# Optimization experiments

Hardware: AMD Instinct MI355X
Metric: run time of the kernel (lower is better)

Reference implementation:

```python
import jax, jax.numpy as jnp
import numpy as np

SEQ, BATCH, IN_DIM, HID, NQ, TAGS = 2048, 1, 8, 4, 4, 32

# ---- 2x2 gate builders (support batched angle t of shape () or (B,)) ----

def _mat2(a, b, c, d):
    vals = [jnp.asarray(v, jnp.complex64) for v in (a, b, c, d)]
    a, b, c, d = jnp.broadcast_arrays(*vals)
    return jnp.stack([jnp.stack([a, b], -1), jnp.stack([c, d], -1)], -2)

def RZg(t):
    t = jnp.asarray(t, jnp.float32).astype(jnp.complex64)
    return _mat2(jnp.exp(-0.5j * t), 0.0, 0.0, jnp.exp(0.5j * t))

def RYg(t):
    t = jnp.asarray(t, jnp.float32); c = jnp.cos(t / 2); s = jnp.sin(t / 2)
    return _mat2(c, -s, s, c)

def RXg(t):
    t = jnp.asarray(t, jnp.float32); c = jnp.cos(t / 2); s = jnp.sin(t / 2)
    return _mat2(c, -1j * s, -1j * s, c)

def PHg(t):
    t = jnp.asarray(t, jnp.float32)
    return _mat2(jnp.ones_like(t), 0.0, 0.0, jnp.exp(1j * t.astype(jnp.complex64)))

_HAD = jnp.array([[1, 1], [1, -1]], jnp.complex64) / np.float32(np.sqrt(2.0))

# ---- statevector primitives (qubit q little-endian: stride 2^q) ----

def apply_1q(psi, U, q, n):
    B = psi.shape[0]
    psi = psi.reshape(B, 1 << (n - 1 - q), 2, 1 << q)
    if U.ndim == 2:
        out = jnp.einsum('ab,Bxby->Bxay', U, psi)
    else:
        out = jnp.einsum('Bab,Bxby->Bxay', U, psi)
    return out.reshape(B, -1)

def apply_cnot(psi, c, t, n):
    B = psi.shape[0]
    p = psi.reshape((B,) + (2,) * n)
    axc, axt = 1 + (n - 1 - c), 1 + (n - 1 - t)
    p = jnp.moveaxis(p, (axc, axt), (1, 2))
    p = jnp.concatenate([p[:, :1], p[:, 1:, ::-1]], axis=1)  # flip target where control=1
    p = jnp.moveaxis(p, (1, 2), (axc, axt))
    return p.reshape(B, -1)

# ---- QCNN conv / pool two-qubit blocks (faithful to source gate lists) ----

def conv_block(psi, a, b, p, n):
    psi = apply_1q(psi, RZg(-np.pi / 2), b, n)
    psi = apply_cnot(psi, b, a, n)
    psi = apply_1q(psi, RZg(p[0]), a, n)
    psi = apply_1q(psi, RYg(p[1]), b, n)
    psi = apply_cnot(psi, a, b, n)
    psi = apply_1q(psi, RYg(p[2]), b, n)
    psi = apply_cnot(psi, b, a, n)
    psi = apply_1q(psi, RZg(np.pi / 2), a, n)
    return psi

def pool_block(psi, a, b, p, n):
    psi = apply_1q(psi, RZg(-np.pi / 2), b, n)
    psi = apply_cnot(psi, b, a, n)
    psi = apply_1q(psi, RZg(p[0]), a, n)
    psi = apply_1q(psi, RYg(p[1]), b, n)
    psi = apply_cnot(psi, a, b, n)
    psi = apply_1q(psi, RYg(p[2]), b, n)
    return psi

# block wiring exactly as built by conv_layer/pool_layer composed on qubits 0..k
CONV1 = [(0, 1), (2, 3), (4, 5), (6, 7), (1, 2), (3, 4), (5, 6), (7, 0)]
POOL1 = [(0, 4), (1, 5), (2, 6), (3, 7)]
CONV2 = [(0, 1), (2, 3), (1, 2), (3, 0)]
POOL2 = [(0, 2), (1, 3)]
CONV3 = [(0, 1), (1, 0)]
POOL3 = [(0, 1)]

def qcnn_forward(x, w):
    # x: (B,8) inputs, w: (63,) ansatz weights -> (B,) expectation <Z_7>
    B = x.shape[0]
    psi = jnp.zeros((B, 256), jnp.complex64).at[:, 0].set(1.0)
    for q in range(8):  # ZFeatureMap(reps=1): H then P(2*x_q) on each qubit
        psi = apply_1q(psi, _HAD, q, 8)
        psi = apply_1q(psi, PHg(2.0 * x[:, q]), q, 8)
    k = 0
    for blocks, fn in ((CONV1, conv_block), (POOL1, pool_block), (CONV2, conv_block),
                       (POOL2, pool_block), (CONV3, conv_block), (POOL3, pool_block)):
        for (a, b) in blocks:
            psi = fn(psi, a, b, w[k:k + 3], 8)
            k += 3
    probs = psi.real ** 2 + psi.imag ** 2
    # observable 'Z'+'I'*7 in Qiskit big-endian string => Z on qubit 7
    sign7 = 1.0 - 2.0 * ((jnp.arange(256) >> 7) & 1).astype(jnp.float32)
    return probs @ sign7

_SIGNS4 = 1.0 - 2.0 * ((jnp.arange(16)[None, :] >> jnp.arange(4)[:, None]) & 1).astype(jnp.float32)  # (4,16)

def qlayer(angles):
    # angles (B,4): encoder rx + trainable rx fused (RX(a)RX(b)=RX(a+b) on same wire)
    B = angles.shape[0]
    psi = jnp.zeros((B, 16), jnp.complex64).at[:, 0].set(1.0)
    for wq in range(4):
        psi = apply_1q(psi, RXg(angles[:, wq]), wq, 4)
    for (c, t) in ((0, 1), (1, 2), (2, 3), (3, 0)):
        psi = apply_cnot(psi, c, t, 4)
    probs = psi.real ** 2 + psi.imag ** 2
    return probs @ _SIGNS4.T  # (B,4) = <Z_w> per wire

def model_forward(sentence, qcnn_w, Wf, bf, Wi, bi, Wu, bu, Wo, bo, thf, thi, thu, tho, Wt, bt):
    S, B, D = sentence.shape
    q = qcnn_forward(sentence.reshape(S * B, D), qcnn_w).reshape(S, B, 1)
    h0 = jnp.zeros((B, HID), jnp.float32)
    c0 = jnp.zeros((B, HID), jnp.float32)
    Ws = jnp.stack([Wf, Wi, Wu, Wo])        # (4, NQ, 1+HID)
    bs = jnp.stack([bf, bi, bu, bo])        # (4, NQ)
    ths = jnp.stack([thf, thi, thu, tho])   # (4, NQ)

    def step(carry, x):
        h, c = carry
        comb = jnp.concatenate([x, h], axis=1)                         # (B, 1+HID)
        ys = jnp.einsum('gqd,Bd->gBq', Ws, comb) + bs[:, None, :]      # (4,B,NQ)
        z = qlayer((ys + ths[:, None, :]).reshape(4 * B, NQ)).reshape(4, B, NQ)
        f = jax.nn.sigmoid(z[0]); i_ = jax.nn.sigmoid(z[1])
        g = jnp.tanh(z[2]); o = jax.nn.sigmoid(z[3])
        c2 = f * c + i_ * g
        h2 = o * jnp.tanh(c2)
        return (h2, c2), h2

    _, hs = jax.lax.scan(step, (h0, c0), q)    # (S,B,HID)
    logits = hs.reshape(S, -1) @ Wt.T + bt      # batch must be 1 per source view()
    return jax.nn.log_softmax(logits, axis=1)


def setup_inputs() -> dict:
    key = jax.random.key(0)
    ks = jax.random.split(key, 16)
    rn = lambda k, s: jax.random.normal(k, s, jnp.float32)
    return {
        'sentence': rn(ks[0], (SEQ, BATCH, IN_DIM)),
        'qcnn_w': rn(ks[1], (63,)),
        'Wf': rn(ks[2], (NQ, 1 + HID)), 'bf': rn(ks[3], (NQ,)),
        'Wi': rn(ks[4], (NQ, 1 + HID)), 'bi': rn(ks[5], (NQ,)),
        'Wu': rn(ks[6], (NQ, 1 + HID)), 'bu': rn(ks[7], (NQ,)),
        'Wo': rn(ks[8], (NQ, 1 + HID)), 'bo': rn(ks[9], (NQ,)),
        'thf': rn(ks[10], (NQ,)), 'thi': rn(ks[11], (NQ,)),
        'thu': rn(ks[12], (NQ,)), 'tho': rn(ks[13], (NQ,)),
        'Wt': rn(ks[14], (TAGS, HID)), 'bt': rn(ks[15], (TAGS,)),
    }


def reference(sentence, qcnn_w, Wf, bf, Wi, bi, Wu, bu, Wo, bo, thf, thi, thu, tho, Wt, bt):
    return model_forward(sentence, qcnn_w, Wf, bf, Wi, bi, Wu, bu, Wo, bo, thf, thi, thu, tho, Wt, bt)
```

## Files before the change

### kernel.cpp

```cpp
#include <hip/hip_runtime.h>
#include <math.h>


#define MAXS 2048
#define SEG  8
#define WARM 24
#define WIN  (WARM + SEG)

__device__ __align__(16) float g_preT[16 * MAXS];

template <int CTRL>
__device__ __forceinline__ float dppf(float x) {
    return __int_as_float(__builtin_amdgcn_update_dpp(
        0, __float_as_int(x), CTRL, 0xF, 0xF, true));
}
#define QP_1032 0xB1
#define QP_2301 0x4E
#define QP_3210 0x1B
#define ROR4  0x124
#define ROR8  0x128
#define ROR12 0x12C

__device__ __forceinline__ float fastrcp(float x) {
    return __builtin_amdgcn_rcpf(x);
}

constexpr int hf(int m)  { return (m ^ (((m << 1) | (m >> 3)) & 15)) & 15; }
__device__ __forceinline__ int swzi(int i) {
    const int m = (i >> 4) & 15;
    return i ^ m ^ (((m << 1) | (m >> 3)) & 15);
}
constexpr int DM(int a) { return (a < 4) ? (1 << a)
                                         : ((1 << a) ^ hf(1 << (a - 4))); }

constexpr int AQ[21] = {0,2,4,6,1,3,5,7, 0,1,2,3, 0,2,1,3, 0,1, 0,1, 0};
constexpr int BQ[21] = {1,3,5,7,2,4,6,0, 4,5,6,7, 1,3,2,0, 2,3, 1,0, 1};
constexpr int CV[21] = {1,1,1,1,1,1,1,1, 0,0,0,0, 1,1,1,1, 0,0, 1,1, 0};

__device__ __forceinline__ float2 cmulacc(float2 acc, float2 u, float2 a) {
    acc.x = fmaf(u.x, a.x, fmaf(-u.y, a.y, acc.x));
    acc.y = fmaf(u.x, a.y, fmaf( u.y, a.x, acc.y));
    return acc;
}

__global__ __launch_bounds__(256) void qcnn_kernel(
    const float* __restrict__ sent, const float* __restrict__ wpar,
    const float* __restrict__ Wf, const float* __restrict__ bfv,
    const float* __restrict__ Wi, const float* __restrict__ bi,
    const float* __restrict__ Wu, const float* __restrict__ bu,
    const float* __restrict__ Wo, const float* __restrict__ bo,
    const float* __restrict__ thf, const float* __restrict__ thi,
    const float* __restrict__ thu, const float* __restrict__ tho, int S)
{
    __shared__ float2 sU[336];
    __shared__ float2 sv[4 * 256];
    const int tid = threadIdx.x;
    const int wid = tid >> 6;
    const int L   = tid & 63;

    if (tid < 84) {
        const int b = tid >> 2, j = tid & 3;
        const float p0 = wpar[3*b], p1 = wpar[3*b+1], p2 = wpar[3*b+2];
        float ur[4] = {0.f,0.f,0.f,0.f}, ui[4] = {0.f,0.f,0.f,0.f};
        ur[j] = 1.f;
        auto rz = [&](int bm, float ch, float sh) {
            #pragma unroll
            for (int m = 0; m < 4; ++m) {
                float pi_ = (m & bm) ? sh : -sh;
                float r  = ur[m]*ch - ui[m]*pi_;
                float im = ur[m]*pi_ + ui[m]*ch;
                ur[m] = r; ui[m] = im;
            }
        };
        auto ry = [&](int bm, float c, float s) {
            #pragma unroll
            for (int m0 = 0; m0 < 4; ++m0) {
                if (m0 & bm) continue;
                int m1 = m0 | bm;
                float r0 = ur[m0], i0 = ui[m0];
                float r1 = ur[m1], i1 = ui[m1];
                ur[m0] = c*r0 - s*r1; ui[m0] = c*i0 - s*i1;
                ur[m1] = s*r0 + c*r1; ui[m1] = s*i0 + c*i1;
            }
        };
        auto sw = [&](int x, int y) {
            float tr = ur[x]; ur[x] = ur[y]; ur[y] = tr;
            float ti = ui[x]; ui[x] = ui[y]; ui[y] = ti;
        };
        const float RT = 0.70710678118654752f;
        float c0,s0,c1,s1,c2,s2;
        __sincosf(0.5f*p0, &s0, &c0);
        __sincosf(0.5f*p1, &s1, &c1);
        __sincosf(0.5f*p2, &s2, &c2);
        rz(2, RT, -RT);
        sw(2, 3);
        rz(1, c0, s0);
        ry(2, c1, s1);
        sw(1, 3);
        ry(2, c2, s2);
        if (CV[b]) { sw(2, 3); rz(1, RT, RT); }
        #pragma unroll
        for (int m = 0; m < 4; ++m)
            sU[(b*4 + m)*4 + j] = make_float2(ur[m], ui[m]);
    }
    __syncthreads();

    int s = blockIdx.x * 4 + wid;
    const bool live = (s < S);
    if (!live) s = S - 1;

    float xs[8];
    #pragma unroll
    for (int q = 0; q < 8; ++q) xs[q] = sent[s * 8 + q];

    float base = 0.f;
    #pragma unroll
    for (int q = 2; q < 8; ++q)
        if ((L >> (q - 2)) & 1) base += xs[q];
    base *= 2.f;
    float2 r[4];
    #pragma unroll
    for (int k = 0; k < 4; ++k) {
        float ph = base;
        if (k & 1) ph += 2.f * xs[0];
        if (k & 2) ph += 2.f * xs[1];
        float sp, cp;
        __sincosf(ph, &sp, &cp);
        r[k] = make_float2(cp * 0.0625f, sp * 0.0625f);
    }

    float2* mysv = sv + wid * 256;
    int si0 = swzi(L * 4);

    #pragma unroll
    for (int blk = 0; blk < 21; ++blk) {
        float2 o[4];
        #pragma unroll
        for (int m = 0; m < 4; ++m) {
            const float4* Urow = (const float4*)(&sU[blk*16 + m*4]);
            float4 u01 = Urow[0];
            float4 u23 = Urow[1];
            float2 acc = make_float2(0.f, 0.f);
            acc = cmulacc(acc, make_float2(u01.x, u01.y), r[0]);
            acc = cmulacc(acc, make_float2(u01.z, u01.w), r[1]);
            acc = cmulacc(acc, make_float2(u23.x, u23.y), r[2]);
            acc = cmulacc(acc, make_float2(u23.z, u23.w), r[3]);
            o[m] = acc;
        }
        #pragma unroll
        for (int m = 0; m < 4; ++m) r[m] = o[m];

        if (blk < 20) {
            const int dA1 = DM(AQ[blk]), dB1 = DM(BQ[blk]);
            mysv[si0            ] = r[0];
            mysv[si0 ^ dA1      ] = r[1];
            mysv[si0 ^ dB1      ] = r[2];
            mysv[si0 ^ dA1 ^ dB1] = r[3];
            __builtin_amdgcn_wave_barrier();
            const int a2 = AQ[blk+1], b2 = BQ[blk+1];
            const int p  = (a2 < b2) ? a2 : b2;
            const int q  = (a2 < b2) ? b2 : a2;
            const int m1 = (1 << p) - 1;
            const int m2 = (1 << (q - 1)) - 1;
            const int i0 = (L & m1) | ((L & (m2 ^ m1)) << 1) | ((L & ~m2) << 2);
            const int si = swzi(i0);
            const int dA2 = DM(a2), dB2 = DM(b2);
            r[0] = mysv[si            ];
            r[1] = mysv[si ^ dA2      ];
            r[2] = mysv[si ^ dB2      ];
            r[3] = mysv[si ^ dA2 ^ dB2];
            __builtin_amdgcn_wave_barrier();
            si0 = si;
        }
    }

    float pr = fmaf(r[0].x, r[0].x, r[0].y * r[0].y)
             + fmaf(r[1].x, r[1].x, r[1].y * r[1].y)
             + fmaf(r[2].x, r[2].x, r[2].y * r[2].y)
             + fmaf(r[3].x, r[3].x, r[3].y * r[3].y);
    if (L >= 32) pr = -pr;
    #pragma unroll
    for (int off = 32; off > 0; off >>= 1)
        pr += __shfl_xor(pr, off, 64);

    if (live && L < 16) {
        const int g = L >> 2, w = L & 3;
        const float* Wg  = (g == 0) ? Wf  : (g == 1) ? Wi  : (g == 2) ? Wu  : Wo;
        const float* bg  = (g == 0) ? bfv : (g == 1) ? bi  : (g == 2) ? bu  : bo;
        const float* thg = (g == 0) ? thf : (g == 1) ? thi : (g == 2) ? thu : tho;
        g_preT[L * MAXS + s] = Wg[w * 5] * pr + bg[w] + thg[w];
    }
}

__global__ __launch_bounds__(64) void lstm_kernel(
    const float* __restrict__ Wf, const float* __restrict__ Wi,
    const float* __restrict__ Wu, const float* __restrict__ Wo,
    const float* __restrict__ Wt, const float* __restrict__ bt,
    float* __restrict__ out, int S)
{
    __shared__ float sW[128];
    __shared__ float sb[32];
    __shared__ float hseg[SEG][4];

    const int b      = blockIdx.x;
    const int tstart = b * SEG;
    if (tstart >= S) return;
    const int tend = (tstart + SEG < S) ? tstart + SEG : S;
    const int t0   = (tstart >= WARM) ? tstart - WARM : 0;

    const int L   = threadIdx.x;
    const int lid = L & 15;
    const int g   = lid >> 2;
    const int w   = lid & 3;

    sW[L] = Wt[L]; sW[64 + L] = Wt[64 + L];
    if (L < 32) sb[L] = bt[L];

    const float* Wg = (g == 0) ? Wf : (g == 1) ? Wi : (g == 2) ? Wu : Wo;
    const float Wp0 = Wg[w*5 + 1 + (w    )];
    const float Wp1 = Wg[w*5 + 1 + (w ^ 1)];
    const float Wp2 = Wg[w*5 + 1 + (w ^ 2)];
    const float Wp3 = Wg[w*5 + 1 + (w ^ 3)];
    const bool  tg  = (g == 2);
    const float selm = tg ? 2.f : 1.f;
    const float adda = tg ? -1.f : 0.f;

    float pres[WIN];
    const float4* rowp = (const float4*)(g_preT + lid * MAXS + t0);
    #pragma unroll
    for (int c = 0; c < WIN/4; ++c) {
        float4 v = rowp[c];
        pres[4*c+0] = v.x; pres[4*c+1] = v.y;
        pres[4*c+2] = v.z; pres[4*c+3] = v.w;
    }

    float hs = 0.f, hb1 = 0.f, hb2 = 0.f, hb3 = 0.f;
    float cst = 0.f;

    #pragma unroll
    for (int k = 0; k < WIN; ++k) {
        const int t = t0 + k;
        float t01 = fmaf(Wp0, hs, Wp1 * hb1);
        float t23 = fmaf(Wp2, hb2, fmaf(Wp3, hb3, pres[k]));
        float th  = t01 + t23;
        float d   = __cosf(th);
        float v1 = dppf<QP_1032>(d);
        float pp = d * v1;
        float v2 = dppf<QP_2301>(pp);
        float z = (w == 0) ? v1 * v2
                : (w == 1) ? pp
                : (w == 2) ? v2 * d
                           : pp * v2;
        float sg = fastrcp(1.f + __expf(-z * selm));
        float a  = fmaf(selm, sg, adda);
        float r4  = dppf<ROR4 >(a);
        float r8  = dppf<ROR8 >(a);
        float r12 = dppf<ROR12>(a);
        float af = (g == 0) ? a : (g == 1) ? r4 : (g == 2) ? r8 : r12;
        float ai = (g == 1) ? a : (g == 2) ? r4 : (g == 3) ? r8 : r12;
        float au = (g == 2) ? a : (g == 3) ? r4 : (g == 0) ? r8 : r12;
        float ao = (g == 3) ? a : (g == 0) ? r4 : (g == 1) ? r8 : r12;
        cst = fmaf(af, cst, ai * au);
        float e2 = __expf(-2.f * cst);
        float hq = ao * fmaf(2.f, fastrcp(1.f + e2), -1.f);
        hs  = hq;
        hb1 = dppf<QP_1032>(hq);
        hb2 = dppf<QP_2301>(hq);
        hb3 = dppf<QP_3210>(hq);
        if (t >= tstart && t < tend && L < 4)
            hseg[t - tstart][L] = hs;
    }

    __builtin_amdgcn_wave_barrier();

    if (L < tend - tstart) {
        const int t = tstart + L;
        const float h0 = hseg[L][0], h1 = hseg[L][1];
        const float h2 = hseg[L][2], h3 = hseg[L][3];
        float lg[32];
        float m = -1e30f;
        #pragma unroll
        for (int j = 0; j < 32; ++j) {
            lg[j] = sW[4*j+0]*h0 + sW[4*j+1]*h1 + sW[4*j+2]*h2
                  + sW[4*j+3]*h3 + sb[j];
            m = fmaxf(m, lg[j]);
        }
        float se = 0.f;
        #pragma unroll
        for (int j = 0; j < 32; ++j) se += __expf(lg[j] - m);
        float lse = m + __logf(se);
        #pragma unroll
        for (int j = 0; j < 32; ++j) out[32*t+j] = lg[j] - lse;
    }
}

extern "C" void kernel_launch(void* const* d_in, const int* in_sizes, int n_in,
                              void* d_out, int out_size, void* d_ws, size_t ws_size,
                              hipStream_t stream)
{
    const float* sent = (const float*)d_in[0];
    const float* wq   = (const float*)d_in[1];
    const float* Wf   = (const float*)d_in[2];  const float* bfv = (const float*)d_in[3];
    const float* Wi   = (const float*)d_in[4];  const float* bi  = (const float*)d_in[5];
    const float* Wu   = (const float*)d_in[6];  const float* bu  = (const float*)d_in[7];
    const float* Wo   = (const float*)d_in[8];  const float* bo  = (const float*)d_in[9];
    const float* thf  = (const float*)d_in[10]; const float* thi = (const float*)d_in[11];
    const float* thu  = (const float*)d_in[12]; const float* tho = (const float*)d_in[13];
    const float* Wt   = (const float*)d_in[14]; const float* bt  = (const float*)d_in[15];

    int S = in_sizes[0] / 8;
    if (S > MAXS) S = MAXS;
    float* outp = (float*)d_out;
    const int nseg = (S + SEG - 1) / SEG;

    qcnn_kernel<<<(S + 3) / 4, 256, 0, stream>>>(sent, wq, Wf, bfv, Wi, bi,
                                                 Wu, bu, Wo, bo,
                                                 thf, thi, thu, tho, S);
    lstm_kernel<<<nseg, 64, 0, stream>>>(Wf, Wi, Wu, Wo, Wt, bt, outp, S);
}
```

Measured before the change: 100.0 us.

## Spread log-softmax epilogue across full wave and hoist qcnn global loads

The LSTM epilogue previously ran the 32-tag projection and log-softmax on only 8 lanes, each doing 32 outputs serially. It now spreads the work over all 64 lanes (8 rows × 8 lanes, 4 tags each), using a padded shared-memory weight layout, shuffle-based max/sum reductions and float4 stores. In the qcnn kernel, the sentence and gate-parameter global loads are hoisted ahead of the unitary-build section and __syncthreads so their latency overlaps that setup. The cost is extra shuffle reductions and a few more registers live across the barrier.

```diff
diff --git a/kernel.cpp b/kernel.cpp
--- a/kernel.cpp
+++ b/kernel.cpp
@@ -58,6 +58,23 @@
     const int wid = tid >> 6;
     const int L   = tid & 63;
 
+    int s = blockIdx.x * 4 + wid;
+    const bool live = (s < S);
+    if (!live) s = S - 1;
+
+    float xs[8];
+    #pragma unroll
+    for (int q = 0; q < 8; ++q) xs[q] = sent[s * 8 + q];
+
+    const int lid = L & 15;
+    const int g   = lid >> 2;
+    const int w   = lid & 3;
+    const float* Wg  = (g == 0) ? Wf  : (g == 1) ? Wi  : (g == 2) ? Wu  : Wo;
+    const float* bg  = (g == 0) ? bfv : (g == 1) ? bi  : (g == 2) ? bu  : bo;
+    const float* thg = (g == 0) ? thf : (g == 1) ? thi : (g == 2) ? thu : tho;
+    const float wsc = Wg[w * 5];
+    const float bth = bg[w] + thg[w];
+
     if (tid < 84) {
         const int b = tid >> 2, j = tid & 3;
         const float p0 = wpar[3*b], p1 = wpar[3*b+1], p2 = wpar[3*b+2];
@@ -72,15 +89,15 @@
                 ur[m] = r; ui[m] = im;
             }
         };
-        auto ry = [&](int bm, float c, float s) {
+        auto ry = [&](int bm, float c, float s_) {
             #pragma unroll
             for (int m0 = 0; m0 < 4; ++m0) {
                 if (m0 & bm) continue;
                 int m1 = m0 | bm;
                 float r0 = ur[m0], i0 = ui[m0];
                 float r1 = ur[m1], i1 = ui[m1];
-                ur[m0] = c*r0 - s*r1; ui[m0] = c*i0 - s*i1;
-                ur[m1] = s*r0 + c*r1; ui[m1] = s*i0 + c*i1;
+                ur[m0] = c*r0 - s_*r1; ui[m0] = c*i0 - s_*i1;
+                ur[m1] = s_*r0 + c*r1; ui[m1] = s_*i0 + c*i1;
             }
         };
         auto sw = [&](int x, int y) {
@@ -104,14 +121,6 @@
             sU[(b*4 + m)*4 + j] = make_float2(ur[m], ui[m]);
     }
     __syncthreads();
-
-    int s = blockIdx.x * 4 + wid;
-    const bool live = (s < S);
-    if (!live) s = S - 1;
-
-    float xs[8];
-    #pragma unroll
-    for (int q = 0; q < 8; ++q) xs[q] = sent[s * 8 + q];
 
     float base = 0.f;
     #pragma unroll
@@ -183,13 +192,8 @@
     for (int off = 32; off > 0; off >>= 1)
         pr += __shfl_xor(pr, off, 64);
 
-    if (live && L < 16) {
-        const int g = L >> 2, w = L & 3;
-        const float* Wg  = (g == 0) ? Wf  : (g == 1) ? Wi  : (g == 2) ? Wu  : Wo;
-        const float* bg  = (g == 0) ? bfv : (g == 1) ? bi  : (g == 2) ? bu  : bo;
-        const float* thg = (g == 0) ? thf : (g == 1) ? thi : (g == 2) ? thu : tho;
-        g_preT[L * MAXS + s] = Wg[w * 5] * pr + bg[w] + thg[w];
-    }
+    if (live && L < 16)
+        g_preT[L * MAXS + s] = wsc * pr + bth;
 }
 
 __global__ __launch_bounds__(64) void lstm_kernel(
@@ -198,7 +202,7 @@
     const float* __restrict__ Wt, const float* __restrict__ bt,
     float* __restrict__ out, int S)
 {
-    __shared__ float sW[128];
+    __shared__ float sWp[192];
     __shared__ float sb[32];
     __shared__ float hseg[SEG][4];
 
@@ -213,8 +217,12 @@
     const int g   = lid >> 2;
     const int w   = lid & 3;
 
-    sW[L] = Wt[L]; sW[64 + L] = Wt[64 + L];
-    if (L < 32) sb[L] = bt[L];
+    {
+        const int i0 = L, i1 = L + 64;
+        sWp[24*(i0 >> 4) + (i0 & 15)] = Wt[i0];
+        sWp[24*(i1 >> 4) + (i1 & 15)] = Wt[i1];
+        if (L < 32) sb[L] = bt[L];
+    }
 
     const float* Wg = (g == 0) ? Wf : (g == 1) ? Wi : (g == 2) ? Wu : Wo;
     const float Wp0 = Wg[w*5 + 1 + (w    )];
@@ -273,24 +281,36 @@
 
     __builtin_amdgcn_wave_barrier();
 
-    if (L < tend - tstart) {
-        const int t = tstart + L;
-        const float h0 = hseg[L][0], h1 = hseg[L][1];
-        const float h2 = hseg[L][2], h3 = hseg[L][3];
-        float lg[32];
-        float m = -1e30f;
-        #pragma unroll
-        for (int j = 0; j < 32; ++j) {
-            lg[j] = sW[4*j+0]*h0 + sW[4*j+1]*h1 + sW[4*j+2]*h2
-                  + sW[4*j+3]*h3 + sb[j];
-            m = fmaxf(m, lg[j]);
+    {
+        const int row = L >> 3;
+        const int j8  = L & 7;
+        const int t   = tstart + row;
+        const float h0 = hseg[row][0], h1 = hseg[row][1];
+        const float h2 = hseg[row][2], h3 = hseg[row][3];
+        const float* wr = &sWp[24 * j8];
+        const float4 w0 = *(const float4*)(wr + 0);
+        const float4 w1 = *(const float4*)(wr + 4);
+        const float4 w2 = *(const float4*)(wr + 8);
+        const float4 w3 = *(const float4*)(wr + 12);
+        const float4 sbv = *(const float4*)(&sb[4 * j8]);
+        float lg0 = fmaf(w0.x,h0, fmaf(w0.y,h1, fmaf(w0.z,h2, fmaf(w0.w,h3, sbv.x))));
+        float lg1 = fmaf(w1.x,h0, fmaf(w1.y,h1, fmaf(w1.z,h2, fmaf(w1.w,h3, sbv.y))));
+        float lg2 = fmaf(w2.x,h0, fmaf(w2.y,h1, fmaf(w2.z,h2, fmaf(w2.w,h3, sbv.z))));
+        float lg3 = fmaf(w3.x,h0, fmaf(w3.y,h1, fmaf(w3.z,h2, fmaf(w3.w,h3, sbv.w))));
+        float m = fmaxf(fmaxf(lg0, lg1), fmaxf(lg2, lg3));
+        #pragma unroll
+        for (int off = 1; off < 8; off <<= 1)
+            m = fmaxf(m, __shfl_xor(m, off, 64));
+        float se = __expf(lg0 - m) + __expf(lg1 - m)
+                 + __expf(lg2 - m) + __expf(lg3 - m);
+        #pragma unroll
+        for (int off = 1; off < 8; off <<= 1)
+            se += __shfl_xor(se, off, 64);
+        const float lse = m + __logf(se);
+        if (t < tend) {
+            float4 ov = make_float4(lg0 - lse, lg1 - lse, lg2 - lse, lg3 - lse);
+            *(float4*)(&out[32*t + 4*j8]) = ov;
         }
-        float se = 0.f;
-        #pragma unroll
-        for (int j = 0; j < 32; ++j) se += __expf(lg[j] - m);
-        float lse = m + __logf(se);
-        #pragma unroll
-        for (int j = 0; j < 32; ++j) out[32*t+j] = lg[j] - lse;
     }
 }
 
```

New measurement: 99.24 us. Within noise of the previous version (-0.8%).
